# Kernel optimization log

Hardware: AMD Instinct MI355X
Metric: run time of the kernel (lower is better)

## Reference

```python
import jax, jax.numpy as jnp
import numpy as np

IOU_POS = 0.5
IOU_NEG = 0.3


def _pairwise_iou(b1, b2):
    # b1: [N,4], b2: [M,4] in xyxy -> [N,M]
    area1 = (b1[:, 2] - b1[:, 0]) * (b1[:, 3] - b1[:, 1])
    area2 = (b2[:, 2] - b2[:, 0]) * (b2[:, 3] - b2[:, 1])
    lt = jnp.maximum(b1[:, None, :2], b2[None, :, :2])
    rb = jnp.minimum(b1[:, None, 2:], b2[None, :, 2:])
    wh = jnp.clip(rb - lt, 0.0)
    inter = wh[..., 0] * wh[..., 1]
    union = area1[:, None] + area2[None, :] - inter
    return inter / jnp.maximum(union, 1e-8)


def _smooth_l1(x):
    ax = jnp.abs(x)
    return jnp.where(ax < 1.0, 0.5 * x * x, ax - 0.5)


def _per_image(cls_o, reg_o, tb, tl):
    # cls_o: [N,C], reg_o: [N,4], tb: [M,4], tl: [M]
    ious = _pairwise_iou(reg_o, tb)            # [N,M]
    max_ious = ious.max(axis=1)
    max_idx = ious.argmax(axis=1)
    pos = max_ious >= IOU_POS
    neg = max_ious < IOU_NEG
    logp = jax.nn.log_softmax(cls_o, axis=-1)  # [N,C]
    matched_lbl = tl[max_idx]                  # [N]
    ce_pos = -jnp.take_along_axis(logp, matched_lbl[:, None], axis=1)[:, 0]
    ce_neg = -logp[:, 0]                       # background class 0
    npos = pos.sum().astype(logp.dtype)
    nneg = neg.sum().astype(logp.dtype)
    cls_loss_pos = jnp.sum(jnp.where(pos, ce_pos, 0.0)) / jnp.maximum(npos, 1.0)
    cls_loss_neg = jnp.sum(jnp.where(neg, ce_neg, 0.0)) / jnp.maximum(nneg, 1.0)
    diff = reg_o - tb[max_idx]                 # [N,4]
    sl1 = _smooth_l1(diff).mean(axis=-1)       # per-anchor mean over 4 coords
    reg_loss = jnp.sum(jnp.where(pos, sl1, 0.0)) / jnp.maximum(npos, 1.0)
    return cls_loss_pos, cls_loss_neg, reg_loss, npos > 0, nneg > 0


def _detection_loss(cls_output, reg_output, target_boxes, target_labels):
    cp, cn, rl, has_p, has_n = jax.vmap(_per_image)(cls_output, reg_output, target_boxes, target_labels)
    cls_vals = jnp.concatenate([cp, cn])
    cls_valid = jnp.concatenate([has_p, has_n]).astype(cls_vals.dtype)
    n_cls = cls_valid.sum()
    cls_mean = jnp.sum(cls_vals * cls_valid) / jnp.maximum(n_cls, 1.0)
    has_pf = has_p.astype(rl.dtype)
    n_reg = has_pf.sum()
    reg_mean = jnp.sum(rl * has_pf) / jnp.maximum(n_reg, 1.0)
    total = jnp.where(n_cls > 0, cls_mean, 0.0) + jnp.where(n_reg > 0, reg_mean, 0.0)
    return total


def setup_inputs() -> dict:
    key = jax.random.key(0)
    k1, k2, k3, k4, k5, k6 = jax.random.split(key, 6)
    B, N, C, M = 8, 131072, 21, 32
    cls_output = jax.random.normal(k1, (B, N, C), dtype=jnp.float32)
    xy = jax.random.uniform(k2, (B, N, 2), minval=0.0, maxval=220.0)
    wh = jax.random.uniform(k3, (B, N, 2), minval=20.0, maxval=80.0)
    reg_output = jnp.concatenate([xy, xy + wh], axis=-1)
    txy = jax.random.uniform(k4, (B, M, 2), minval=0.0, maxval=220.0)
    twh = jax.random.uniform(k5, (B, M, 2), minval=20.0, maxval=80.0)
    target_boxes = jnp.concatenate([txy, txy + twh], axis=-1)
    target_labels = jax.random.randint(k6, (B, M), 1, C)
    return {"cls_output": cls_output, "reg_output": reg_output,
            "target_boxes": target_boxes, "target_labels": target_labels}


def reference(cls_output, reg_output, target_boxes, target_labels):
    return _detection_loss(cls_output, reg_output, target_boxes, target_labels)
```

## Files before the change

kernel.cpp:

```cpp
#include <hip/hip_runtime.h>
#include <math.h>

#define TPB 256
#define NC 21
#define NM 32

__global__ __launch_bounds__(TPB) void detloss_main(
    const float* __restrict__ cls, const float* __restrict__ reg,
    const float* __restrict__ tbx, const int* __restrict__ tlb,
    float* __restrict__ partials, int N, int nblk)
{
    __shared__ float4 s_tb4[NM];
    __shared__ float  s_area2[NM];
    __shared__ int    s_tl[NM];
    __shared__ float  s_red[TPB / 64][5];

    const int t   = threadIdx.x;
    const int blk = blockIdx.x;
    const int b   = blockIdx.y;
    const int row = blk * TPB + t;

    if (t < NM) {
        const float4 tb = ((const float4*)tbx)[(size_t)b * NM + t];
        s_tb4[t]   = tb;
        s_area2[t] = (tb.z - tb.x) * (tb.w - tb.y);
        s_tl[t]    = tlb[(size_t)b * NM + t];
    }
    __syncthreads();

    float v0 = 0.f, v1 = 0.f, v2 = 0.f, v3 = 0.f, v4 = 0.f;
    if (row < N) {
        const float4 rg = ((const float4*)reg)[(size_t)b * N + row];
        const float a1 = (rg.z - rg.x) * (rg.w - rg.y);

        float bi, bu; int bidx = 0;
        {
            const float4 tb = s_tb4[0];
            const float lx = fmaxf(rg.x, tb.x), ly = fmaxf(rg.y, tb.y);
            const float rx = fminf(rg.z, tb.z), ry = fminf(rg.w, tb.w);
            const float w  = fmaxf(rx - lx, 0.f), h = fmaxf(ry - ly, 0.f);
            bi = w * h;
            bu = a1 + s_area2[0] - bi;
        }
        #pragma unroll
        for (int j = 1; j < NM; ++j) {
            const float4 tb = s_tb4[j];
            const float lx = fmaxf(rg.x, tb.x), ly = fmaxf(rg.y, tb.y);
            const float rx = fminf(rg.z, tb.z), ry = fminf(rg.w, tb.w);
            const float w  = fmaxf(rx - lx, 0.f), h = fmaxf(ry - ly, 0.f);
            const float inter = w * h;
            const float uni   = a1 + s_area2[j] - inter;
            const bool  gt    = inter * bu > bi * uni;
            bi   = gt ? inter : bi;
            bu   = gt ? uni   : bu;
            bidx = gt ? j     : bidx;
        }
        const bool pos = (bi >= 0.5f * bu);
        const bool neg = (bi <  0.3f * bu);
        const int  lbl = s_tl[bidx];

        const char* xg = (const char*)(cls + ((size_t)b * N + row) * NC);
        float s0 = 0.f, s1 = 0.f, s2 = 0.f, s3 = 0.f;
        float x0 = 0.f, xlbl = 0.f;
        #pragma unroll
        for (int i = 0; i < 5; ++i) {
            float4 v;
            __builtin_memcpy(&v, xg + 16 * i, 16);
            s0 += __expf(v.x); s1 += __expf(v.y);
            s2 += __expf(v.z); s3 += __expf(v.w);
            if (i == 0) x0 = v.x;
            const int base = 4 * i;
            const float sel = (lbl == base    ) ? v.x :
                              (lbl == base + 1) ? v.y :
                              (lbl == base + 2) ? v.z : v.w;
            xlbl = (lbl >= base && lbl <= base + 3) ? sel : xlbl;
        }
        {
            float xl;
            __builtin_memcpy(&xl, xg + 80, 4);
            s0 += __expf(xl);
            xlbl = (lbl == 20) ? xl : xlbl;
        }
        const float lse    = __logf((s0 + s1) + (s2 + s3));
        const float ce_pos = lse - xlbl;
        const float ce_neg = lse - x0;

        const float4 mb = s_tb4[bidx];
        float rr[4] = {rg.x, rg.y, rg.z, rg.w};
        float mm[4] = {mb.x, mb.y, mb.z, mb.w};
        float sl = 0.f;
        #pragma unroll
        for (int k = 0; k < 4; ++k) {
            const float d  = rr[k] - mm[k];
            const float ad = fabsf(d);
            sl += (ad < 1.0f) ? 0.5f * d * d : (ad - 0.5f);
        }
        sl *= 0.25f;

        if (pos) { v0 = ce_pos; v2 = sl; v3 = 1.f; }
        if (neg) { v1 = ce_neg; v4 = 1.f; }
    }

    #pragma unroll
    for (int o = 32; o > 0; o >>= 1) {
        v0 += __shfl_down(v0, o);
        v1 += __shfl_down(v1, o);
        v2 += __shfl_down(v2, o);
        v3 += __shfl_down(v3, o);
        v4 += __shfl_down(v4, o);
    }
    const int wave = t >> 6;
    if ((t & 63) == 0) {
        s_red[wave][0] = v0; s_red[wave][1] = v1; s_red[wave][2] = v2;
        s_red[wave][3] = v3; s_red[wave][4] = v4;
    }
    __syncthreads();
    if (t == 0) {
        float r0 = 0, r1 = 0, r2 = 0, r3 = 0, r4 = 0;
        #pragma unroll
        for (int w = 0; w < TPB / 64; ++w) {
            r0 += s_red[w][0]; r1 += s_red[w][1]; r2 += s_red[w][2];
            r3 += s_red[w][3]; r4 += s_red[w][4];
        }
        float* q = partials + ((size_t)b * nblk + blk) * 5;
        q[0] = r0; q[1] = r1; q[2] = r2; q[3] = r3; q[4] = r4;
    }
}

__global__ __launch_bounds__(512) void detloss_final(
    const float* __restrict__ partials, int nblk, int B, float* __restrict__ out)
{
    __shared__ float s_img[8][5];
    const int t    = threadIdx.x;
    const int b    = t >> 6;
    const int lane = t & 63;

    if (b < B) {
        float v[5] = {0.f, 0.f, 0.f, 0.f, 0.f};
        for (int e = lane; e < nblk; e += 64) {
            const float* q = partials + ((size_t)b * nblk + e) * 5;
            #pragma unroll
            for (int k = 0; k < 5; ++k) v[k] += q[k];
        }
        #pragma unroll
        for (int o = 32; o > 0; o >>= 1) {
            #pragma unroll
            for (int k = 0; k < 5; ++k) v[k] += __shfl_down(v[k], o);
        }
        if (lane == 0) {
            const float npos = v[3], nneg = v[4];
            s_img[b][0] = v[0] / fmaxf(npos, 1.f);
            s_img[b][1] = v[1] / fmaxf(nneg, 1.f);
            s_img[b][2] = v[2] / fmaxf(npos, 1.f);
            s_img[b][3] = (npos > 0.f) ? 1.f : 0.f;
            s_img[b][4] = (nneg > 0.f) ? 1.f : 0.f;
        }
    }
    __syncthreads();

    if (t == 0) {
        float cls_sum = 0.f, n_cls = 0.f, reg_sum = 0.f, n_reg = 0.f;
        for (int b2 = 0; b2 < B; ++b2) {
            cls_sum += s_img[b2][0] * s_img[b2][3] + s_img[b2][1] * s_img[b2][4];
            n_cls   += s_img[b2][3] + s_img[b2][4];
            reg_sum += s_img[b2][2] * s_img[b2][3];
            n_reg   += s_img[b2][3];
        }
        const float cls_mean = cls_sum / fmaxf(n_cls, 1.f);
        const float reg_mean = reg_sum / fmaxf(n_reg, 1.f);
        out[0] = ((n_cls > 0.f) ? cls_mean : 0.f) + ((n_reg > 0.f) ? reg_mean : 0.f);
    }
}

extern "C" void kernel_launch(void* const* d_in, const int* in_sizes, int n_in,
                              void* d_out, int out_size, void* d_ws, size_t ws_size,
                              hipStream_t stream) {
    const float* cls = (const float*)d_in[0];
    const float* reg = (const float*)d_in[1];
    const float* tbx = (const float*)d_in[2];
    const int*   tlb = (const int*)d_in[3];
    float*       out = (float*)d_out;
    float*  partials = (float*)d_ws;

    const int B = 8;
    const int N = in_sizes[1] / (B * 4);
    const int nblk = (N + TPB - 1) / TPB;

    dim3 grid(nblk, B);
    detloss_main<<<grid, TPB, 0, stream>>>(cls, reg, tbx, tlb, partials, N, nblk);
    detloss_final<<<1, 512, 0, stream>>>(partials, nblk, B, out);
}
```

Before: 35.95 us.

## Stage class logits through shared memory with coalesced float4 loads overlapping IoU

Each block now loads its contiguous 256x21 slab of class logits with fully coalesced float4 loads into registers, issued before the IoU argmax loop so the global latency overlaps that compute. The staged values are then written to shared memory and each thread reads its own row from LDS for the log-sum-exp. This replaces strided, unaligned per-thread 84-byte row loads. In exchange it uses about 21 KB of LDS per block, which may reduce occupancy, and the stride-21 LDS reads may cause bank conflicts.

```diff
diff --git a/kernel.cpp b/kernel.cpp
--- a/kernel.cpp
+++ b/kernel.cpp
@@ -13,12 +13,14 @@
     __shared__ float4 s_tb4[NM];
     __shared__ float  s_area2[NM];
     __shared__ int    s_tl[NM];
+    __shared__ float  s_cls[TPB * NC];
     __shared__ float  s_red[TPB / 64][5];
 
-    const int t   = threadIdx.x;
-    const int blk = blockIdx.x;
-    const int b   = blockIdx.y;
-    const int row = blk * TPB + t;
+    const int t    = threadIdx.x;
+    const int blk  = blockIdx.x;
+    const int b    = blockIdx.y;
+    const int row0 = blk * TPB;
+    const int row  = row0 + t;
 
     if (t < NM) {
         const float4 tb = ((const float4*)tbx)[(size_t)b * NM + t];
@@ -26,80 +28,99 @@
         s_area2[t] = (tb.z - tb.x) * (tb.w - tb.y);
         s_tl[t]    = tlb[(size_t)b * NM + t];
     }
-    __syncthreads();
-
-    float v0 = 0.f, v1 = 0.f, v2 = 0.f, v3 = 0.f, v4 = 0.f;
-    if (row < N) {
-        const float4 rg = ((const float4*)reg)[(size_t)b * N + row];
-        const float a1 = (rg.z - rg.x) * (rg.w - rg.y);
-
-        float bi, bu; int bidx = 0;
-        {
-            const float4 tb = s_tb4[0];
-            const float lx = fmaxf(rg.x, tb.x), ly = fmaxf(rg.y, tb.y);
-            const float rx = fminf(rg.z, tb.z), ry = fminf(rg.w, tb.w);
-            const float w  = fmaxf(rx - lx, 0.f), h = fmaxf(ry - ly, 0.f);
-            bi = w * h;
-            bu = a1 + s_area2[0] - bi;
-        }
-        #pragma unroll
-        for (int j = 1; j < NM; ++j) {
-            const float4 tb = s_tb4[j];
-            const float lx = fmaxf(rg.x, tb.x), ly = fmaxf(rg.y, tb.y);
-            const float rx = fminf(rg.z, tb.z), ry = fminf(rg.w, tb.w);
-            const float w  = fmaxf(rx - lx, 0.f), h = fmaxf(ry - ly, 0.f);
-            const float inter = w * h;
-            const float uni   = a1 + s_area2[j] - inter;
-            const bool  gt    = inter * bu > bi * uni;
-            bi   = gt ? inter : bi;
-            bu   = gt ? uni   : bu;
-            bidx = gt ? j     : bidx;
-        }
-        const bool pos = (bi >= 0.5f * bu);
-        const bool neg = (bi <  0.3f * bu);
-        const int  lbl = s_tl[bidx];
-
-        const char* xg = (const char*)(cls + ((size_t)b * N + row) * NC);
-        float s0 = 0.f, s1 = 0.f, s2 = 0.f, s3 = 0.f;
-        float x0 = 0.f, xlbl = 0.f;
-        #pragma unroll
-        for (int i = 0; i < 5; ++i) {
-            float4 v;
-            __builtin_memcpy(&v, xg + 16 * i, 16);
-            s0 += __expf(v.x); s1 += __expf(v.y);
-            s2 += __expf(v.z); s3 += __expf(v.w);
-            if (i == 0) x0 = v.x;
-            const int base = 4 * i;
-            const float sel = (lbl == base    ) ? v.x :
-                              (lbl == base + 1) ? v.y :
-                              (lbl == base + 2) ? v.z : v.w;
-            xlbl = (lbl >= base && lbl <= base + 3) ? sel : xlbl;
-        }
-        {
-            float xl;
-            __builtin_memcpy(&xl, xg + 80, 4);
-            s0 += __expf(xl);
-            xlbl = (lbl == 20) ? xl : xlbl;
-        }
-        const float lse    = __logf((s0 + s1) + (s2 + s3));
-        const float ce_pos = lse - xlbl;
-        const float ce_neg = lse - x0;
-
-        const float4 mb = s_tb4[bidx];
-        float rr[4] = {rg.x, rg.y, rg.z, rg.w};
-        float mm[4] = {mb.x, mb.y, mb.z, mb.w};
-        float sl = 0.f;
-        #pragma unroll
-        for (int k = 0; k < 4; ++k) {
-            const float d  = rr[k] - mm[k];
-            const float ad = fabsf(d);
-            sl += (ad < 1.0f) ? 0.5f * d * d : (ad - 0.5f);
-        }
+
+    const int rows = min(TPB, N - row0);
+    const float* cls_base = cls + ((size_t)b * N + row0) * NC;
+    const bool fastpath = (rows == TPB) && ((((size_t)cls_base) & 15) == 0);
+    float4 stg[6];
+    const int total4 = TPB * NC / 4;
+    if (fastpath) {
+        const float4* s4 = (const float4*)cls_base;
+        #pragma unroll
+        for (int r = 0; r < 6; ++r) {
+            const int i = r * TPB + t;
+            if (i < total4) stg[r] = s4[i];
+        }
+    }
+
+    const int   rowi = (row < N) ? row : (N - 1);
+    const float msk  = (row < N) ? 1.f : 0.f;
+    const float4 rg  = ((const float4*)reg)[(size_t)b * N + rowi];
+
+    __syncthreads();
+
+    const float a1 = (rg.z - rg.x) * (rg.w - rg.y);
+    float bi, bu; int bidx = 0;
+    {
+        const float4 tb = s_tb4[0];
+        const float lx = fmaxf(rg.x, tb.x), ly = fmaxf(rg.y, tb.y);
+        const float rx = fminf(rg.z, tb.z), ry = fminf(rg.w, tb.w);
+        const float w  = fmaxf(rx - lx, 0.f), h = fmaxf(ry - ly, 0.f);
+        bi = w * h;
+        bu = a1 + s_area2[0] - bi;
+    }
+    #pragma unroll
+    for (int j = 1; j < NM; ++j) {
+        const float4 tb = s_tb4[j];
+        const float lx = fmaxf(rg.x, tb.x), ly = fmaxf(rg.y, tb.y);
+        const float rx = fminf(rg.z, tb.z), ry = fminf(rg.w, tb.w);
+        const float w  = fmaxf(rx - lx, 0.f), h = fmaxf(ry - ly, 0.f);
+        const float inter = w * h;
+        const float uni   = a1 + s_area2[j] - inter;
+        const bool  gt    = inter * bu > bi * uni;
+        bi   = gt ? inter : bi;
+        bu   = gt ? uni   : bu;
+        bidx = gt ? j     : bidx;
+    }
+    const bool pos = (bi >= 0.5f * bu);
+    const bool neg = (bi <  0.3f * bu);
+    const int  lbl = s_tl[bidx];
+
+    if (fastpath) {
+        float4* d4 = (float4*)s_cls;
+        #pragma unroll
+        for (int r = 0; r < 6; ++r) {
+            const int i = r * TPB + t;
+            if (i < total4) d4[i] = stg[r];
+        }
+    } else {
+        for (int i = t; i < TPB * NC; i += TPB)
+            s_cls[i] = (i < rows * NC) ? cls_base[i] : 0.f;
+    }
+    __syncthreads();
+
+    const float* xr = &s_cls[t * NC];
+    float s0 = 0.f, s1 = 0.f, s2 = 0.f, s3 = 0.f;
+    #pragma unroll
+    for (int i = 0; i < 5; ++i) {
+        float4 v;
+        __builtin_memcpy(&v, (const char*)xr + 16 * i, 16);
+        s0 += __expf(v.x); s1 += __expf(v.y);
+        s2 += __expf(v.z); s3 += __expf(v.w);
+    }
+    s0 += __expf(xr[20]);
+    const float lse    = __logf((s0 + s1) + (s2 + s3));
+    const float ce_pos = lse - xr[lbl];
+    const float ce_neg = lse - xr[0];
+
+    const float4 mb = s_tb4[bidx];
+    float sl = 0.f;
+    {
+        const float d0 = rg.x - mb.x, d1 = rg.y - mb.y;
+        const float d2 = rg.z - mb.z, d3 = rg.w - mb.w;
+        const float e0 = fabsf(d0), e1 = fabsf(d1);
+        const float e2 = fabsf(d2), e3 = fabsf(d3);
+        sl += (e0 < 1.f) ? 0.5f * d0 * d0 : (e0 - 0.5f);
+        sl += (e1 < 1.f) ? 0.5f * d1 * d1 : (e1 - 0.5f);
+        sl += (e2 < 1.f) ? 0.5f * d2 * d2 : (e2 - 0.5f);
+        sl += (e3 < 1.f) ? 0.5f * d3 * d3 : (e3 - 0.5f);
         sl *= 0.25f;
-
-        if (pos) { v0 = ce_pos; v2 = sl; v3 = 1.f; }
-        if (neg) { v1 = ce_neg; v4 = 1.f; }
-    }
+    }
+
+    const float pm = (pos ? 1.f : 0.f) * msk;
+    const float nm = (neg ? 1.f : 0.f) * msk;
+    float v0 = pm * ce_pos, v2 = pm * sl, v3 = pm;
+    float v1 = nm * ce_neg, v4 = nm;
 
     #pragma unroll
     for (int o = 32; o > 0; o >>= 1) {
```

Measured after the change: 55.61 us. 54.7% more time.
